# Optimization experiments

Measured on AMD Instinct MI355X. Metric: run time of the kernel, lower is better.

Reference implementation:

```python
import jax, jax.numpy as jnp
import numpy as np

# Dims: T time steps (PoissonEncoder seq_length=50), batch B, input N_IN, hidden H, labels L
T, B, N_IN, H, L = 50, 1024, 784, 256, 10
DT = 0.001            # norse default dt
TAU_SYN_INV = 100.0   # 1/0.01
TAU_MEM_INV = 50.0    # 1/0.02
V_LEAK, V_TH, V_RESET = 0.0, 0.5, 0.0
ALPHA = 100.0         # SuperSpike surrogate slope

@jax.custom_vjp
def superspike(x):
    # Heaviside forward, SuperSpike surrogate backward (norse 'super' method)
    return (x > 0).astype(x.dtype)

def _ss_fwd(x):
    return superspike(x), x

def _ss_bwd(x, g):
    return (g / (ALPHA * jnp.abs(x) + 1.0) ** 2,)

superspike.defvjp(_ss_fwd, _ss_bwd)

def setup_inputs() -> dict:
    key = jax.random.key(0)
    ks = jax.random.split(key, 5)
    # Poisson-encoded spike train, time-major [T, B, N_IN]
    x = (jax.random.uniform(ks[0], (T, B, N_IN)) < 0.3).astype(jnp.float32)
    Wi = jax.random.normal(ks[1], (H, N_IN), dtype=jnp.float32) / np.float32(np.sqrt(N_IN))
    Wr = jax.random.normal(ks[2], (H, H), dtype=jnp.float32) / np.float32(np.sqrt(H))
    Wout = jax.random.normal(ks[3], (L, H), dtype=jnp.float32) / np.float32(np.sqrt(H))
    bout = jnp.zeros((L,), dtype=jnp.float32)
    return {"x": x, "Wi": Wi, "Wr": Wr, "Wout": Wout, "bout": bout}

def reference(x, Wi, Wr, Wout, bout):
    Tw, Bb, _ = x.shape
    Hh = Wi.shape[0]
    Ll = Wout.shape[0]
    z0 = jnp.zeros((Bb, Hh), x.dtype)
    acc0 = jnp.zeros((Bb, Ll), x.dtype)

    def step(carry, x_t):
        z, v, i, acc = carry
        # LIF dynamics (norse lif_step)
        v_dec = v + DT * TAU_MEM_INV * ((V_LEAK - v) + i)   # voltage integration
        i_dec = i * (1.0 - DT * TAU_SYN_INV)                # synaptic current decay
        z_new = superspike(v_dec - V_TH)                    # spike
        v_new = (1.0 - z_new) * v_dec + z_new * V_RESET     # reset
        i_new = i_dec + x_t @ Wi.T + z @ Wr.T               # input + recurrent drive
        # per-step readout accumulation
        acc = acc + z_new @ Wout.T + bout
        return (z_new, v_new, i_new, acc), None

    (_, _, _, acc), _ = jax.lax.scan(step, (z0, z0, z0, acc0), x)
    return acc / Tw  # outputs.float() / time_window (is_test=False path)
```

## Files before the change

### kernel.cpp

```cpp
#include <hip/hip_runtime.h>
#include <cstdint>
#include <cstddef>

#define T_STEPS 50
#define B_SZ    1024
#define N_INP   784
#define H_SZ    256
#define L_SZ    10
#define M_TOT   (T_STEPS * B_SZ)
#define NK0     26
#define NSLICE  5

typedef int v4i  __attribute__((ext_vector_type(4)));
typedef int v16i __attribute__((ext_vector_type(16)));

__global__ __launch_bounds__(256) void transpose_wr(const float* __restrict__ Wr,
                                                    float* __restrict__ WrTz) {
    __shared__ float tile[32][33];
    int bx = blockIdx.x * 32, by = blockIdx.y * 32;
    int tx = threadIdx.x % 32, ty = threadIdx.x / 32;
    #pragma unroll
    for (int j = 0; j < 32; j += 8)
        tile[ty + j][tx] = Wr[(size_t)(by + ty + j) * H_SZ + bx + tx];
    __syncthreads();
    #pragma unroll
    for (int j = 0; j < 32; j += 8)
        WrTz[(size_t)(bx + ty + j) * H_SZ + by + tx] = tile[tx][ty + j];
}

__global__ __launch_bounds__(128) void prep_packed(const float* __restrict__ Wi,
                                                   uint8_t* __restrict__ SBp) {
    const int nt   = blockIdx.x;
    const int k0   = blockIdx.y * 2 + (threadIdx.x >> 6);
    const int lane = threadIdx.x & 63;
    const int h    = nt * 32 + (lane & 31);
    const int g    = k0 * 2 + (lane >> 5);

    int wd[NSLICE][4] = {};
    #pragma unroll
    for (int u = 0; u < 16; ++u) {
        double wv = 0.0;
        if (g < 49) wv = (double)Wi[(size_t)h * N_INP + g * 16 + u];
        double r = rint(wv * 0x1p40);
        #pragma unroll
        for (int j = 0; j < NSLICE - 1; ++j) {
            double q  = floor((r + 128.0) * 0.00390625);
            double dj = r - 256.0 * q;
            wd[j][u >> 2] |= ((int)dj & 0xFF) << ((u & 3) * 8);
            r = q;
        }
        wd[NSLICE - 1][u >> 2] |= ((int)r & 0xFF) << ((u & 3) * 8);
    }
    uint8_t* base = SBp + ((size_t)(nt * NK0 + k0) * NSLICE) * 1024 + lane * 16;
    #pragma unroll
    for (int j = 0; j < NSLICE; ++j)
        *(v4i*)(base + (size_t)j * 1024) = (v4i){wd[j][0], wd[j][1], wd[j][2], wd[j][3]};
}

__global__ __launch_bounds__(256) void pack_x(const float* __restrict__ X,
                                              uint8_t* __restrict__ Ap) {
    const int mt  = blockIdx.x;
    const int tid = threadIdx.x;
    #pragma unroll
    for (int i = 0; i < 7; ++i) {
        int s = tid + i * 256;
        if (s < NK0 * 64) {
            int k0 = s >> 6, lane = s & 63;
            int m = mt * 32 + (lane & 31);
            int g = k0 * 2 + (lane >> 5);
            unsigned int bw[4] = {0u, 0u, 0u, 0u};
            if (g < 49) {
                const float* src = X + (size_t)m * N_INP + g * 16;
                #pragma unroll
                for (int q = 0; q < 4; ++q) {
                    float4 f = *(const float4*)(src + q * 4);
                    bw[q] = (f.x != 0.f ? 1u : 0u) | (f.y != 0.f ? 0x100u : 0u)
                          | (f.z != 0.f ? 0x10000u : 0u) | (f.w != 0.f ? 0x1000000u : 0u);
                }
            }
            *(v4i*)(Ap + ((size_t)(mt * NK0 + k0)) * 1024 + lane * 16) =
                (v4i){(int)bw[0], (int)bw[1], (int)bw[2], (int)bw[3]};
        }
    }
}

__global__ __launch_bounds__(256) void gemm_i8s(const uint8_t* __restrict__ Ap,
                                                const uint8_t* __restrict__ SBp,
                                                double* __restrict__ cur) {
    __shared__ __align__(16) uint8_t Bs[2][2 * NSLICE * 1024];

    const int tid   = threadIdx.x;
    const int wave  = tid >> 6;
    const int lane  = tid & 63;
    const int ghalf = lane >> 5;
    const int nt    = blockIdx.y;
    const int mt0   = (blockIdx.x * 4 + wave) * 2;
    const int mt1   = mt0 + 1;

    const uint8_t* ap0 = Ap + (size_t)mt0 * NK0 * 1024 + lane * 16;
    const uint8_t* ap1 = Ap + (size_t)mt1 * NK0 * 1024 + lane * 16;
    const uint8_t* bbase = SBp + ((size_t)nt * NK0 * NSLICE) * 1024;

    {
        const uint8_t* src = bbase;
        #pragma unroll
        for (int i = 0; i < 2; ++i) {
            int s = tid + i * 256;
            *(v4i*)(Bs[0] + s * 16) = *(const v4i*)(src + s * 16);
        }
        if (tid < 128) {
            int s = tid + 512;
            *(v4i*)(Bs[0] + s * 16) = *(const v4i*)(src + s * 16);
        }
    }
    v4i a0c = *(const v4i*)(ap0);
    v4i a0n = *(const v4i*)(ap0 + 1024);
    v4i a1c = *(const v4i*)(ap1);
    v4i a1n = *(const v4i*)(ap1 + 1024);
    __syncthreads();

    v16i acc0[NSLICE] = {};
    v16i acc1[NSLICE] = {};

    for (int p = 0; p < 13; ++p) {
        const int cb = p & 1;
        v4i b0c = a0c, b0n = a0n, b1c = a1c, b1n = a1n;
        if (p < 12) {
            const uint8_t* src = bbase + (size_t)(p + 1) * 2 * NSLICE * 1024;
            uint8_t* dst = Bs[cb ^ 1];
            #pragma unroll
            for (int i = 0; i < 2; ++i) {
                int s = tid + i * 256;
                *(v4i*)(dst + s * 16) = *(const v4i*)(src + s * 16);
            }
            if (tid < 128) {
                int s = tid + 512;
                *(v4i*)(dst + s * 16) = *(const v4i*)(src + s * 16);
            }
            a0c = *(const v4i*)(ap0 + (size_t)(2 * p + 2) * 1024);
            a0n = *(const v4i*)(ap0 + (size_t)(2 * p + 3) * 1024);
            a1c = *(const v4i*)(ap1 + (size_t)(2 * p + 2) * 1024);
            a1n = *(const v4i*)(ap1 + (size_t)(2 * p + 3) * 1024);
        }
        #pragma unroll
        for (int dk = 0; dk < 2; ++dk) {
            v4i aa0 = dk ? b0n : b0c;
            v4i aa1 = dk ? b1n : b1c;
            #pragma unroll
            for (int j = 0; j < NSLICE; ++j) {
                v4i b = *(const v4i*)(Bs[cb] + (dk * NSLICE + j) * 1024 + lane * 16);
                acc0[j] = __builtin_amdgcn_mfma_i32_32x32x32_i8(aa0, b, acc0[j], 0, 0, 0);
                acc1[j] = __builtin_amdgcn_mfma_i32_32x32x32_i8(aa1, b, acc1[j], 0, 0, 0);
            }
        }
        __syncthreads();
    }

    const int h = nt * 32 + (lane & 31);
    #pragma unroll
    for (int r = 0; r < 16; ++r) {
        int mloc = (r & 3) + 8 * (r >> 2) + 4 * ghalf;
        double s0 = (double)acc0[4][r];
        s0 = s0 * 256.0 + (double)acc0[3][r];
        s0 = s0 * 256.0 + (double)acc0[2][r];
        s0 = s0 * 256.0 + (double)acc0[1][r];
        s0 = s0 * 256.0 + (double)acc0[0][r];
        cur[(size_t)(mt0 * 32 + mloc) * H_SZ + h] = s0 * 0x1p-40;
        double s1 = (double)acc1[4][r];
        s1 = s1 * 256.0 + (double)acc1[3][r];
        s1 = s1 * 256.0 + (double)acc1[2][r];
        s1 = s1 * 256.0 + (double)acc1[1][r];
        s1 = s1 * 256.0 + (double)acc1[0][r];
        cur[(size_t)(mt1 * 32 + mloc) * H_SZ + h] = s1 * 0x1p-40;
    }
}

__device__ __forceinline__ int build_list_pad(const unsigned long long* zm, int h,
                                              int* list) {
    unsigned long long w0 = zm[0], w1 = zm[1], w2 = zm[2], w3 = zm[3];
    int c0 = __popcll(w0), c1 = __popcll(w1), c2 = __popcll(w2), c3 = __popcll(w3);
    int wi = h >> 6;
    unsigned long long word = zm[wi];
    int base = (wi > 0 ? c0 : 0) + (wi > 1 ? c1 : 0) + (wi > 2 ? c2 : 0);
    int bit = h & 63;
    bool act = (word >> bit) & 1ull;
    int pos = __popcll(word & ((1ull << bit) - 1ull));
    if (act) list[base + pos] = h;
    int tot = c0 + c1 + c2 + c3;
    if (h < 8) list[tot + h] = 256;
    return tot;
}

__global__ __launch_bounds__(256) void snn_scan(const double* __restrict__ cur,
                                                const float* __restrict__ WrTz,
                                                const float* __restrict__ Wout,
                                                const float* __restrict__ bout,
                                                float* __restrict__ out) {
    const int b = blockIdx.x;
    const int h = threadIdx.x;

    __shared__ unsigned long long zmS[4];
    __shared__ int listS[2][H_SZ + 8];
    __shared__ float cntS[H_SZ];

    double v = 0.0, syn = 0.0;
    int cnt = 0;
    int nn[2] = {0, 0};

    const double* curb = cur + (size_t)b * H_SZ + h;
    const float*  wrh  = WrTz + h;
    double inp_c = curb[0];

    for (int t = 0; t < T_STEPS; ++t) {
        const int p = t & 1;
        int tn = (t < T_STEPS - 1) ? t + 1 : t;
        double inp_n = curb[(size_t)tn * B_SZ * H_SZ];

        double v_dec = v + 0.05 * ((0.0 - v) + syn);
        double i_dec = 0.9 * syn;
        bool   z_new = v_dec > 0.5;
        v = z_new ? 0.0 : v_dec;
        cnt += z_new ? 1 : 0;

        double r0 = 0.0, r1 = 0.0, r2 = 0.0, r3 = 0.0;
        const int* lp = listS[p];
        const int  n  = nn[p];
        for (int j = 0; j < n; j += 8) {
            float f0 = wrh[(size_t)lp[j + 0] * H_SZ];
            float f1 = wrh[(size_t)lp[j + 1] * H_SZ];
            float f2 = wrh[(size_t)lp[j + 2] * H_SZ];
            float f3 = wrh[(size_t)lp[j + 3] * H_SZ];
            float f4 = wrh[(size_t)lp[j + 4] * H_SZ];
            float f5 = wrh[(size_t)lp[j + 5] * H_SZ];
            float f6 = wrh[(size_t)lp[j + 6] * H_SZ];
            float f7 = wrh[(size_t)lp[j + 7] * H_SZ];
            r0 += (double)f0 + (double)f1;
            r1 += (double)f2 + (double)f3;
            r2 += (double)f4 + (double)f5;
            r3 += (double)f6 + (double)f7;
        }

        unsigned long long bal = __ballot((int)z_new);
        if ((h & 63) == 0) zmS[h >> 6] = bal;
        __syncthreads();
        nn[p ^ 1] = build_list_pad(zmS, h, listS[p ^ 1]);
        syn = (i_dec + inp_c) + ((r0 + r1) + (r2 + r3));
        inp_c = inp_n;
        __syncthreads();
    }

    cntS[h] = (float)cnt;
    __syncthreads();
    if (h < L_SZ) {
        double s = 0.0;
        for (int k = 0; k < H_SZ; ++k)
            s += (double)cntS[k] * (double)Wout[(size_t)h * H_SZ + k];
        s += (double)T_STEPS * (double)bout[h];
        out[(size_t)b * L_SZ + h] = (float)(s / (double)T_STEPS);
    }
}

extern "C" void kernel_launch(void* const* d_in, const int* in_sizes, int n_in,
                              void* d_out, int out_size, void* d_ws, size_t ws_size,
                              hipStream_t stream) {
    const float* x    = (const float*)d_in[0];
    const float* Wi   = (const float*)d_in[1];
    const float* Wr   = (const float*)d_in[2];
    const float* Wout = (const float*)d_in[3];
    const float* bout = (const float*)d_in[4];
    float* out = (float*)d_out;

    char* ws = (char*)d_ws;
    double*  cur  = (double*)(ws);
    float*   WrTz = (float*)(ws + 104857600);
    uint8_t* SBp  = (uint8_t*)(ws + 105121792);
    uint8_t* Ap   = (uint8_t*)(ws + 106186752);

    hipMemsetAsync(WrTz + 256 * H_SZ, 0, H_SZ * sizeof(float), stream);
    hipLaunchKernelGGL(transpose_wr, dim3(8, 8), dim3(256), 0, stream, Wr, WrTz);
    hipLaunchKernelGGL(prep_packed, dim3(8, 13), dim3(128), 0, stream, Wi, SBp);
    hipLaunchKernelGGL(pack_x, dim3(M_TOT / 32), dim3(256), 0, stream, x, Ap);
    hipLaunchKernelGGL(gemm_i8s, dim3(M_TOT / 256, 8), dim3(256), 0, stream, Ap, SBp, cur);
    hipLaunchKernelGGL(snn_scan, dim3(B_SZ), dim3(256), 0, stream,
                       cur, WrTz, Wout, bout, out);
}
```

Before: 404.3 us.

## Keep A tiles in registers and loop over four N tiles per block

The int8 GEMM now loads each wave's full K strip of packed input spikes into registers once and reuses it across four output column tiles. Blocks shrink to two waves, and the grid changes from (200,8) to (400,2). The aim is to cut repeated global reads of the large packed A matrix, which was previously re-read for every N tile. The cost is heavy register pressure (52 v4i of A plus accumulators), reduced occupancy under launch_bounds(128,1), and B tiles being refetched into LDS per N tile.

```diff
diff --git a/kernel.cpp b/kernel.cpp
--- a/kernel.cpp
+++ b/kernel.cpp
@@ -84,94 +84,87 @@
     }
 }
 
-__global__ __launch_bounds__(256) void gemm_i8s(const uint8_t* __restrict__ Ap,
-                                                const uint8_t* __restrict__ SBp,
-                                                double* __restrict__ cur) {
+__global__ __launch_bounds__(128, 1) void gemm_i8r(const uint8_t* __restrict__ Ap,
+                                                   const uint8_t* __restrict__ SBp,
+                                                   double* __restrict__ cur) {
     __shared__ __align__(16) uint8_t Bs[2][2 * NSLICE * 1024];
 
     const int tid   = threadIdx.x;
     const int wave  = tid >> 6;
     const int lane  = tid & 63;
     const int ghalf = lane >> 5;
-    const int nt    = blockIdx.y;
-    const int mt0   = (blockIdx.x * 4 + wave) * 2;
+    const int mt0   = (blockIdx.x * 2 + wave) * 2;
     const int mt1   = mt0 + 1;
-
-    const uint8_t* ap0 = Ap + (size_t)mt0 * NK0 * 1024 + lane * 16;
-    const uint8_t* ap1 = Ap + (size_t)mt1 * NK0 * 1024 + lane * 16;
-    const uint8_t* bbase = SBp + ((size_t)nt * NK0 * NSLICE) * 1024;
-
+    const int ntq   = blockIdx.y * 4;
+
+    v4i a0[NK0], a1[NK0];
     {
-        const uint8_t* src = bbase;
-        #pragma unroll
-        for (int i = 0; i < 2; ++i) {
-            int s = tid + i * 256;
-            *(v4i*)(Bs[0] + s * 16) = *(const v4i*)(src + s * 16);
-        }
-        if (tid < 128) {
-            int s = tid + 512;
-            *(v4i*)(Bs[0] + s * 16) = *(const v4i*)(src + s * 16);
-        }
-    }
-    v4i a0c = *(const v4i*)(ap0);
-    v4i a0n = *(const v4i*)(ap0 + 1024);
-    v4i a1c = *(const v4i*)(ap1);
-    v4i a1n = *(const v4i*)(ap1 + 1024);
-    __syncthreads();
-
-    v16i acc0[NSLICE] = {};
-    v16i acc1[NSLICE] = {};
-
-    for (int p = 0; p < 13; ++p) {
-        const int cb = p & 1;
-        v4i b0c = a0c, b0n = a0n, b1c = a1c, b1n = a1n;
-        if (p < 12) {
-            const uint8_t* src = bbase + (size_t)(p + 1) * 2 * NSLICE * 1024;
-            uint8_t* dst = Bs[cb ^ 1];
+        const uint8_t* ap0 = Ap + (size_t)mt0 * NK0 * 1024 + lane * 16;
+        const uint8_t* ap1 = Ap + (size_t)mt1 * NK0 * 1024 + lane * 16;
+        #pragma unroll
+        for (int k0 = 0; k0 < NK0; ++k0) {
+            a0[k0] = *(const v4i*)(ap0 + (size_t)k0 * 1024);
+            a1[k0] = *(const v4i*)(ap1 + (size_t)k0 * 1024);
+        }
+    }
+
+    for (int nti = 0; nti < 4; ++nti) {
+        const int nt = ntq + nti;
+        const uint8_t* bbase = SBp + ((size_t)nt * NK0 * NSLICE) * 1024;
+
+        #pragma unroll
+        for (int i = 0; i < 5; ++i) {
+            int s = tid + i * 128;
+            *(v4i*)(Bs[0] + s * 16) = *(const v4i*)(bbase + s * 16);
+        }
+        __syncthreads();
+
+        v16i acc0[NSLICE] = {};
+        v16i acc1[NSLICE] = {};
+
+        #pragma unroll
+        for (int p = 0; p < 13; ++p) {
+            const int cb = p & 1;
+            if (p < 12) {
+                const uint8_t* src = bbase + (size_t)(p + 1) * 2 * NSLICE * 1024;
+                uint8_t* dst = Bs[cb ^ 1];
+                #pragma unroll
+                for (int i = 0; i < 5; ++i) {
+                    int s = tid + i * 128;
+                    *(v4i*)(dst + s * 16) = *(const v4i*)(src + s * 16);
+                }
+            }
             #pragma unroll
-            for (int i = 0; i < 2; ++i) {
-                int s = tid + i * 256;
-                *(v4i*)(dst + s * 16) = *(const v4i*)(src + s * 16);
+            for (int dk = 0; dk < 2; ++dk) {
+                v4i aa0 = a0[p * 2 + dk];
+                v4i aa1 = a1[p * 2 + dk];
+                #pragma unroll
+                for (int j = 0; j < NSLICE; ++j) {
+                    v4i b = *(const v4i*)(Bs[cb] + (dk * NSLICE + j) * 1024 + lane * 16);
+                    acc0[j] = __builtin_amdgcn_mfma_i32_32x32x32_i8(aa0, b, acc0[j], 0, 0, 0);
+                    acc1[j] = __builtin_amdgcn_mfma_i32_32x32x32_i8(aa1, b, acc1[j], 0, 0, 0);
+                }
             }
-            if (tid < 128) {
-                int s = tid + 512;
-                *(v4i*)(dst + s * 16) = *(const v4i*)(src + s * 16);
-            }
-            a0c = *(const v4i*)(ap0 + (size_t)(2 * p + 2) * 1024);
-            a0n = *(const v4i*)(ap0 + (size_t)(2 * p + 3) * 1024);
-            a1c = *(const v4i*)(ap1 + (size_t)(2 * p + 2) * 1024);
-            a1n = *(const v4i*)(ap1 + (size_t)(2 * p + 3) * 1024);
-        }
-        #pragma unroll
-        for (int dk = 0; dk < 2; ++dk) {
-            v4i aa0 = dk ? b0n : b0c;
-            v4i aa1 = dk ? b1n : b1c;
-            #pragma unroll
-            for (int j = 0; j < NSLICE; ++j) {
-                v4i b = *(const v4i*)(Bs[cb] + (dk * NSLICE + j) * 1024 + lane * 16);
-                acc0[j] = __builtin_amdgcn_mfma_i32_32x32x32_i8(aa0, b, acc0[j], 0, 0, 0);
-                acc1[j] = __builtin_amdgcn_mfma_i32_32x32x32_i8(aa1, b, acc1[j], 0, 0, 0);
-            }
-        }
-        __syncthreads();
-    }
-
-    const int h = nt * 32 + (lane & 31);
-    #pragma unroll
-    for (int r = 0; r < 16; ++r) {
-        int mloc = (r & 3) + 8 * (r >> 2) + 4 * ghalf;
-        double s0 = (double)acc0[4][r];
-        s0 = s0 * 256.0 + (double)acc0[3][r];
-        s0 = s0 * 256.0 + (double)acc0[2][r];
-        s0 = s0 * 256.0 + (double)acc0[1][r];
-        s0 = s0 * 256.0 + (double)acc0[0][r];
-        cur[(size_t)(mt0 * 32 + mloc) * H_SZ + h] = s0 * 0x1p-40;
-        double s1 = (double)acc1[4][r];
-        s1 = s1 * 256.0 + (double)acc1[3][r];
-        s1 = s1 * 256.0 + (double)acc1[2][r];
-        s1 = s1 * 256.0 + (double)acc1[1][r];
-        s1 = s1 * 256.0 + (double)acc1[0][r];
-        cur[(size_t)(mt1 * 32 + mloc) * H_SZ + h] = s1 * 0x1p-40;
+            __syncthreads();
+        }
+
+        const int h = nt * 32 + (lane & 31);
+        #pragma unroll
+        for (int r = 0; r < 16; ++r) {
+            int mloc = (r & 3) + 8 * (r >> 2) + 4 * ghalf;
+            double s0 = (double)acc0[4][r];
+            s0 = s0 * 256.0 + (double)acc0[3][r];
+            s0 = s0 * 256.0 + (double)acc0[2][r];
+            s0 = s0 * 256.0 + (double)acc0[1][r];
+            s0 = s0 * 256.0 + (double)acc0[0][r];
+            cur[(size_t)(mt0 * 32 + mloc) * H_SZ + h] = s0 * 0x1p-40;
+            double s1 = (double)acc1[4][r];
+            s1 = s1 * 256.0 + (double)acc1[3][r];
+            s1 = s1 * 256.0 + (double)acc1[2][r];
+            s1 = s1 * 256.0 + (double)acc1[1][r];
+            s1 = s1 * 256.0 + (double)acc1[0][r];
+            cur[(size_t)(mt1 * 32 + mloc) * H_SZ + h] = s1 * 0x1p-40;
+        }
     }
 }
 
@@ -280,7 +273,7 @@
     hipLaunchKernelGGL(transpose_wr, dim3(8, 8), dim3(256), 0, stream, Wr, WrTz);
     hipLaunchKernelGGL(prep_packed, dim3(8, 13), dim3(128), 0, stream, Wi, SBp);
     hipLaunchKernelGGL(pack_x, dim3(M_TOT / 32), dim3(256), 0, stream, x, Ap);
-    hipLaunchKernelGGL(gemm_i8s, dim3(M_TOT / 256, 8), dim3(256), 0, stream, Ap, SBp, cur);
+    hipLaunchKernelGGL(gemm_i8r, dim3(400, 2), dim3(128), 0, stream, Ap, SBp, cur);
     hipLaunchKernelGGL(snn_scan, dim3(B_SZ), dim3(256), 0, stream,
                        cur, WrTz, Wout, bout, out);
 }
```

Result: slower. 530.1 us (+31.1%).
